# Kernel optimization log

Measured on AMD Instinct MI355X. Metric: run time of the kernel, lower is better.

## Reference

```python
import jax, jax.numpy as jnp
import numpy as np

C = 128
N_ATOMS = 3584          # 512 * 7 bands
DILATIONS = (1, 3, 9, 27, 81, 1)
NEG = 0.2               # leaky_relu slope used throughout the repo
B, T = 8, 2048


def lrelu(x):
    return jnp.where(x >= 0, x, NEG * x)


def setup_inputs() -> dict:
    key = jax.random.key(0)
    keys = iter(jax.random.split(key, 40))

    def rn(shape, scale=0.05):
        return jax.random.normal(next(keys), shape, jnp.float32) * scale

    # x: [B, 4, T]; channel 0 = atom index (stored as float, cast with .long() in forward),
    # channels 1:3 = (pos, amp), channel 3 = band size (unused by forward)
    atoms = jax.random.randint(next(keys), (B, 1, T), 0, N_ATOMS).astype(jnp.float32)
    pos_amp = jax.random.normal(next(keys), (B, 2, T), jnp.float32)
    band = jnp.zeros((B, 1, T), jnp.float32)
    x = jnp.concatenate([atoms, pos_amp, band], axis=1)

    nl = len(DILATIONS)
    return {
        "x": x,
        "embed_w": rn((N_ATOMS, C), 0.1),
        "posamp_w": rn((C, 2), 0.1), "posamp_b": jnp.zeros((C,), jnp.float32),
        "reduce_w": rn((C, 2 * C)), "reduce_b": jnp.zeros((C,), jnp.float32),
        "dil_w": rn((nl, C, C, 3)), "dil_b": jnp.zeros((nl, C), jnp.float32),
        "one_w": rn((nl, C, C)), "one_b": jnp.zeros((nl, C), jnp.float32),
        "atom_w1": rn((C, C)), "atom_b1": jnp.zeros((C,), jnp.float32),
        "atom_w2": rn((C, C)), "atom_b2": jnp.zeros((C,), jnp.float32),
        "atom_w3": rn((N_ATOMS, C)), "atom_b3": jnp.zeros((N_ATOMS,), jnp.float32),
        "pa_w1": rn((C, C)), "pa_b1": jnp.zeros((C,), jnp.float32),
        "pa_w2": rn((C, C)), "pa_b2": jnp.zeros((C,), jnp.float32),
        "pa_w3": rn((2, C)), "pa_b3": jnp.zeros((2,), jnp.float32),
    }


def _linear_stack(h, w1, b1, w2, b2, w3, b3):
    # LinearOutputStack(channels, 3, out_channels=...): two hidden linears with
    # leaky_relu, final linear with no activation.
    h = lrelu(h @ w1.T + b1)
    h = lrelu(h @ w2.T + b2)
    return h @ w3.T + b3


def reference(x, embed_w, posamp_w, posamp_b, reduce_w, reduce_b,
              dil_w, dil_b, one_w, one_b,
              atom_w1, atom_b1, atom_w2, atom_b2, atom_w3, atom_b3,
              pa_w1, pa_b1, pa_w2, pa_b2, pa_w3, pa_b3):
    xt = jnp.transpose(x, (0, 2, 1))                              # [B,T,4]
    idx = jax.lax.stop_gradient(xt[:, :, 0]).astype(jnp.int32)    # atom ids
    at = embed_w[idx]                                             # [B,T,C] gather
    pa = xt[:, :, 1:3] @ posamp_w.T + posamp_b                    # [B,T,C]
    h = jnp.concatenate([at, pa], axis=-1)                        # [B,T,2C]
    h = h @ reduce_w.T + reduce_b                                 # 1x1 conv == linear
    h = jnp.transpose(h, (0, 2, 1))                               # [B,C,T]

    # DilatedStack: residual blocks (dilated k=3 conv -> 1x1 conv -> +res -> lrelu)
    for i, d in enumerate(DILATIONS):
        orig = h
        y = jax.lax.conv_general_dilated(
            h, dil_w[i], window_strides=(1,), padding=[(d, d)],
            rhs_dilation=(d,), dimension_numbers=('NCH', 'OIH', 'NCH'))
        y = y + dil_b[i][None, :, None]
        y = jnp.einsum('oc,bct->bot', one_w[i], y) + one_b[i][None, :, None]
        h = lrelu(y + orig)

    ht = jnp.transpose(h, (0, 2, 1))                              # [B,T,C]
    # Original applies the output stacks over all T, then slices the last step.
    a = _linear_stack(ht, atom_w1, atom_b1, atom_w2, atom_b2, atom_w3, atom_b3)[:, -1:, :]
    pa_out = _linear_stack(ht, pa_w1, pa_b1, pa_w2, pa_b2, pa_w3, pa_b3)[:, -1:, :]
    return a, pa_out
```

## Files before the change

### kernel.cpp

```cpp
#include <hip/hip_runtime.h>

#define CCH 128
#define TLEN 2048
#define NBATCH 8
#define NATOMS 3584
#define NEG 0.2f
typedef unsigned long long ull;

#define PK1(a) ((ull)(a))
#define PK2(a,b) (PK1(a)|((ull)(b)<<7))
#define PK3(a,b,c) (PK2(a,b)|((ull)(c)<<14))
#define PK4(a,b,c,d) (PK3(a,b,c)|((ull)(d)<<21))
#define PK5(a,b,c,d,e) (PK4(a,b,c,d)|((ull)(e)<<28))
#define P6(v,k) ((ull)(v)<<(6*(k)))
#define PX10(a,b,c,d,e,f,g,h,i,j) (P6(a,0)|P6(b,1)|P6(c,2)|P6(d,3)|P6(e,4)| \
    P6(f,5)|P6(g,6)|P6(h,7)|P6(i,8)|P6(j,9))

__device__ const int g_l2cols[28] = {
    9,10,18,19,27,28,36,37,45,46,54,55,63,64,
    72,73,81,82,90,91,99,100,108,109,117,118,126,127};

__device__ __forceinline__ float lrelu(float v) { return v >= 0.f ? v : NEG * v; }
__device__ __forceinline__ float dot4(float4 w, float4 x) {
    return w.x * x.x + w.y * x.y + w.z * x.z + w.w * x.w;
}

__device__ __forceinline__ void warm(const float* p, int nf4, int gid, int nthr) {
    const float4* q = (const float4*)p;
    for (int i = gid; i < nf4; i += nthr) {
        float4 v = q[i];
        asm volatile("" :: "v"(v.x), "v"(v.y), "v"(v.z), "v"(v.w));
    }
}

__device__ __forceinline__ float red16x4(float a0, float a1, float a2, float a3, int s) {
    a0 += __shfl_xor(a0, 8); a1 += __shfl_xor(a1, 8);
    a2 += __shfl_xor(a2, 8); a3 += __shfl_xor(a3, 8);
    a0 += __shfl_xor(a0, 4); a1 += __shfl_xor(a1, 4);
    a2 += __shfl_xor(a2, 4); a3 += __shfl_xor(a3, 4);
    float u0 = (s & 2) ? a2 : a0;
    float v0 = (s & 2) ? a0 : a2;
    u0 += __shfl_xor(v0, 2);
    float u1 = (s & 2) ? a3 : a1;
    float v1 = (s & 2) ? a1 : a3;
    u1 += __shfl_xor(v1, 2);
    float w  = (s & 1) ? u1 : u0;
    float vv = (s & 1) ? u0 : u1;
    w += __shfl_xor(vv, 1);
    return w;
}

template<int NB, int SH = 7>
__device__ __forceinline__ void conv4(
        const float (*src)[CCH], float (*dst)[CCH], float* gout,
        ull pm, ull pc, ull pp, ull pd, int a0,
        const float* __restrict__ Wd, const float* __restrict__ bd,
        const float* __restrict__ Wo, const float* __restrict__ bo,
        float (*ybuf)[CCH], int g, int s)
{
    const int MSK = (1 << SH) - 1;
    const int ch = 4 * g + (s & 3);
    const float myBd = bd[ch];
    const float myBo = bo[ch];
    float4 W[24], V[8];
    {
        const float4* Wr = (const float4*)Wd + (size_t)(4 * g) * 96;
        #pragma unroll
        for (int r = 0; r < 4; ++r)
            #pragma unroll
            for (int j = 0; j < 3; ++j) {
                W[r * 6 + j]     = Wr[r * 96 + 3 * s + j];
                W[r * 6 + 3 + j] = Wr[r * 96 + 3 * s + 48 + j];
            }
        const float4* Or = (const float4*)Wo + (size_t)(4 * g) * 32;
        #pragma unroll
        for (int r = 0; r < 4; ++r) {
            V[r * 2]     = Or[r * 32 + s];
            V[r * 2 + 1] = Or[r * 32 + s + 16];
        }
    }
    __syncthreads();
    #pragma unroll
    for (int t = 0; t < NB; ++t) {
        const float* fm = src[(int)((pm >> (SH * t)) & MSK)];
        const float* fc = src[(int)((pc >> (SH * t)) & MSK)];
        const float* fp = src[(int)((pp >> (SH * t)) & MSK)];
        float4 m0 = *(const float4*)(fm + 4 * s);
        float4 m1 = *(const float4*)(fm + 4 * s + 64);
        float4 c0 = *(const float4*)(fc + 4 * s);
        float4 c1 = *(const float4*)(fc + 4 * s + 64);
        float4 p0 = *(const float4*)(fp + 4 * s);
        float4 p1 = *(const float4*)(fp + 4 * s + 64);
        float acc[4];
        #pragma unroll
        for (int r = 0; r < 4; ++r) {
            float4 wA = W[r*6+0], wB = W[r*6+1], wC = W[r*6+2];
            float a = wA.x*m0.x + wA.y*c0.x + wA.z*p0.x + wA.w*m0.y
                    + wB.x*c0.y + wB.y*p0.y + wB.z*m0.z + wB.w*c0.z
                    + wC.x*p0.z + wC.y*m0.w + wC.z*c0.w + wC.w*p0.w;
            float4 wD = W[r*6+3], wE = W[r*6+4], wF = W[r*6+5];
            float b2 = wD.x*m1.x + wD.y*c1.x + wD.z*p1.x + wD.w*m1.y
                     + wE.x*c1.y + wE.y*p1.y + wE.z*m1.z + wE.w*c1.z
                     + wF.x*p1.z + wF.y*m1.w + wF.z*c1.w + wF.w*p1.w;
            acc[r] = a + b2;
        }
        float tot = red16x4(acc[0], acc[1], acc[2], acc[3], s);
        if (s < 4) ybuf[t][ch] = tot + myBd;
    }
    __syncthreads();
    #pragma unroll
    for (int t = 0; t < NB; ++t) {
        int jc = (int)((pc >> (SH * t)) & MSK);
        int jd = (int)((pd >> (SH * t)) & MSK);
        const float* y = ybuf[t];
        float4 y0 = *(const float4*)(y + 4 * s);
        float4 y1 = *(const float4*)(y + 4 * s + 64);
        float a0_ = dot4(V[0], y0) + dot4(V[1], y1);
        float a1_ = dot4(V[2], y0) + dot4(V[3], y1);
        float a2_ = dot4(V[4], y0) + dot4(V[5], y1);
        float a3_ = dot4(V[6], y0) + dot4(V[7], y1);
        float tot = red16x4(a0_, a1_, a2_, a3_, s);
        if (s < 4) {
            float h = lrelu(tot + myBo + src[jc][ch]);
            if (gout) gout[ch] = h;
            else      dst[jd][ch] = (a0 + jd < 128) ? h : 0.f;
        }
    }
}

__device__ __forceinline__ void mlp4(
        const float* hin, float* hout,
        const float* __restrict__ w, const float* __restrict__ bv,
        int g, int s)
{
    const int ch = 4 * g + (s & 3);
    const float myB = bv[ch];
    float4 V[8];
    const float4* r = (const float4*)w + (size_t)(4 * g) * 32;
    #pragma unroll
    for (int rr = 0; rr < 4; ++rr) {
        V[rr * 2]     = r[rr * 32 + s];
        V[rr * 2 + 1] = r[rr * 32 + s + 16];
    }
    __syncthreads();
    float4 x0 = *(const float4*)(hin + 4 * s);
    float4 x1 = *(const float4*)(hin + 4 * s + 64);
    float a0_ = dot4(V[0], x0) + dot4(V[1], x1);
    float a1_ = dot4(V[2], x0) + dot4(V[3], x1);
    float a2_ = dot4(V[4], x0) + dot4(V[5], x1);
    float a3_ = dot4(V[6], x0) + dot4(V[7], x1);
    float tot = red16x4(a0_, a1_, a2_, a3_, s);
    if (s < 4) hout[ch] = lrelu(tot + myB);
}

__global__ void __launch_bounds__(512, 2) k_cone(
        const float* __restrict__ x,
        const float* __restrict__ embed_w,
        const float* __restrict__ posamp_w,
        const float* __restrict__ posamp_b,
        const float* __restrict__ reduce_w,
        const float* __restrict__ reduce_b,
        const float* __restrict__ dil_w,
        const float* __restrict__ dil_b,
        const float* __restrict__ one_w,
        const float* __restrict__ one_b,
        const float* __restrict__ aw1, const float* __restrict__ aw2,
        const float* __restrict__ pw1, const float* __restrict__ pw2,
        const float* __restrict__ aw3,
        float* __restrict__ l2c)
{
    const int i   = blockIdx.x;
    const int b   = blockIdx.y;
    const int own = g_l2cols[i];
    const int a0  = own - 4;
    const int tid = threadIdx.x;
    const int g   = tid >> 4;
    const int s   = tid & 15;
    const int ch  = 4 * g + (s & 3);

    {
        const int gid  = (b * 28 + i) * 512 + tid;
        const int nthr = 224 * 512;
        warm(dil_w + (size_t)2 * CCH * CCH * 3, 4 * CCH * CCH * 3 / 4, gid, nthr);
        warm(one_w + (size_t)2 * CCH * CCH,     4 * CCH * CCH / 4,     gid, nthr);
        warm(aw1, CCH * CCH / 4, gid, nthr);
        warm(aw2, CCH * CCH / 4, gid, nthr);
        warm(pw1, CCH * CCH / 4, gid, nthr);
        warm(pw2, CCH * CCH / 4, gid, nthr);
        warm(aw3, NATOMS * CCH / 4, gid, nthr);
    }

    __shared__ float A[9][CCH];
    __shared__ float B[8][CCH];
    __shared__ float cat[9][2 * CCH];
    __shared__ float ybuf[3][CCH];

    const float* xb = x + b * 4 * TLEN;
    for (int v = tid; v < 9 * 256; v += 512) {
        int p   = v >> 8;
        int chv = v & 255;
        int ab  = a0 + p;
        float val = 0.f;
        if (ab < 128) {
            int t = (TLEN - 128) + ab;
            if (chv < CCH) {
                int idx = (int)xb[t];
                val = embed_w[idx * CCH + chv];
            } else {
                int cc = chv - CCH;
                val = posamp_w[2 * cc] * xb[TLEN + t]
                    + posamp_w[2 * cc + 1] * xb[2 * TLEN + t] + posamp_b[cc];
            }
        }
        cat[p][chv] = val;
    }
    float4 RW[16];
    const float4* rw = (const float4*)reduce_w + (size_t)(4 * g) * 64;
    #pragma unroll
    for (int r = 0; r < 4; ++r)
        #pragma unroll
        for (int j = 0; j < 4; ++j)
            RW[r * 4 + j] = rw[r * 64 + s + 16 * j];
    const float rb = reduce_b[ch];
    __syncthreads();

    #pragma unroll 3
    for (int t = 0; t < 9; ++t) {
        const float* sc = cat[t];
        float4 x0 = *(const float4*)(sc + 4 * s);
        float4 x1 = *(const float4*)(sc + 4 * s + 64);
        float4 x2 = *(const float4*)(sc + 4 * s + 128);
        float4 x3 = *(const float4*)(sc + 4 * s + 192);
        float a0_ = dot4(RW[0], x0) + dot4(RW[1], x1) + dot4(RW[2], x2) + dot4(RW[3], x3);
        float a1_ = dot4(RW[4], x0) + dot4(RW[5], x1) + dot4(RW[6], x2) + dot4(RW[7], x3);
        float a2_ = dot4(RW[8], x0) + dot4(RW[9], x1) + dot4(RW[10], x2) + dot4(RW[11], x3);
        float a3_ = dot4(RW[12], x0) + dot4(RW[13], x1) + dot4(RW[14], x2) + dot4(RW[15], x3);
        float tot = red16x4(a0_, a1_, a2_, a3_, s);
        if (s < 4) A[t][ch] = (a0 + t < 128) ? tot + rb : 0.f;
    }

    conv4<3>(A, B, nullptr,
             PK3(0,3,6), PK3(1,4,7), PK3(2,5,8), PK3(1,4,7), a0,
             dil_w, dil_b, one_w, one_b, ybuf, g, s);
    conv4<1>(B, B, l2c + (size_t)(b * 28 + i) * CCH,
             PK1(1), PK1(4), PK1(7), PK1(4), a0,
             dil_w + (size_t)1 * CCH * CCH * 3, dil_b + CCH,
             one_w + (size_t)1 * CCH * CCH, one_b + CCH, ybuf, g, s);
}

__global__ void __launch_bounds__(512, 2) k_tail(
        const float* __restrict__ l2c,
        const float* __restrict__ dil_w,
        const float* __restrict__ dil_b,
        const float* __restrict__ one_w,
        const float* __restrict__ one_b,
        const float* __restrict__ aw1, const float* __restrict__ ab1,
        const float* __restrict__ aw2, const float* __restrict__ ab2,
        const float* __restrict__ aw3, const float* __restrict__ ab3,
        const float* __restrict__ pw1, const float* __restrict__ pb1,
        const float* __restrict__ pw2, const float* __restrict__ pb2,
        const float* __restrict__ pw3, const float* __restrict__ pb3,
        float* __restrict__ out)
{
    const int g2  = blockIdx.x;
    const int b   = blockIdx.y;
    const int tid = threadIdx.x;
    const int g   = tid >> 4;
    const int s   = tid & 15;

    __shared__ float E[29][CCH];
    __shared__ float D[11][CCH];
    __shared__ float B2[5][CCH];
    __shared__ float C2[3][CCH];
    __shared__ float HF[CCH];
    __shared__ float ybuf[10][CCH];
    __shared__ float h1a[CCH], h2a[CCH], h1p[CCH], h2p[CCH];

    if (tid < CCH) { E[28][tid] = 0.f; D[10][tid] = 0.f; B2[4][tid] = 0.f; C2[2][tid] = 0.f; }
    for (int v = tid; v < 28 * 32; v += 512) {
        int col = v >> 5, f4i = v & 31;
        *(float4*)&E[col][f4i * 4] =
            *(const float4*)(l2c + (size_t)(b * 28 + col) * CCH + f4i * 4);
    }

    conv4<10, 6>(E, D, nullptr,
             PX10(0,1,6,7,12,13,18,19,24,25),
             PX10(2,3,8,9,14,15,20,21,26,27),
             PX10(4,5,10,11,16,17,22,23,28,28),
             PX10(0,1,2,3,4,5,6,7,8,9), -1000,
             dil_w + (size_t)2 * CCH * CCH * 3, dil_b + 2 * CCH,
             one_w + (size_t)2 * CCH * CCH, one_b + 2 * CCH, ybuf, g, s);

    conv4<4>(D, B2, nullptr,
             PK4(0,1,6,7), PK4(2,3,8,9), PK4(4,5,10,10), PK4(0,1,2,3), -1000,
             dil_w + (size_t)3 * CCH * CCH * 3, dil_b + 3 * CCH,
             one_w + (size_t)3 * CCH * CCH, one_b + 3 * CCH, ybuf, g, s);
    conv4<2>(B2, C2, nullptr,
             PK2(0,1), PK2(2,3), PK2(4,4), PK2(0,1), -1000,
             dil_w + (size_t)4 * CCH * CCH * 3, dil_b + 4 * CCH,
             one_w + (size_t)4 * CCH * CCH, one_b + 4 * CCH, ybuf, g, s);
    conv4<1>(C2, C2, HF,
             PK1(0), PK1(1), PK1(2), PK1(0), -1000,
             dil_w + (size_t)5 * CCH * CCH * 3, dil_b + 5 * CCH,
             one_w + (size_t)5 * CCH * CCH, one_b + 5 * CCH, ybuf, g, s);

    mlp4(HF, h1a, aw1, ab1, g, s);
    mlp4(HF, h1p, pw1, pb1, g, s);
    mlp4(h1a, h2a, aw2, ab2, g, s);
    mlp4(h1p, h2p, pw2, pb2, g, s);
    __syncthreads();

    if (tid < 448) {
        int row = g2 * 448 + tid;
        const float4* r = (const float4*)(aw3 + (size_t)row * CCH);
        float s0 = 0.f, s1 = 0.f, s2 = 0.f, s3 = 0.f;
        #pragma unroll
        for (int k = 0; k < 32; k += 4) {
            s0 += dot4(r[k],     *(const float4*)&h2a[4 * k]);
            s1 += dot4(r[k + 1], *(const float4*)&h2a[4 * k + 4]);
            s2 += dot4(r[k + 2], *(const float4*)&h2a[4 * k + 8]);
            s3 += dot4(r[k + 3], *(const float4*)&h2a[4 * k + 12]);
        }
        out[b * NATOMS + row] = s0 + s1 + s2 + s3 + ab3[row];
    } else if (g2 == 0 && tid >= 448 && tid < 448 + 64) {
        int q = tid - 448;
        int row = q >> 5, qq = q & 31;
        float4 w4 = *(const float4*)(pw3 + row * CCH + 4 * qq);
        float4 xv = *(const float4*)(h2p + 4 * qq);
        float acc = dot4(w4, xv);
        acc += __shfl_xor(acc, 1);
        acc += __shfl_xor(acc, 2);
        acc += __shfl_xor(acc, 4);
        acc += __shfl_xor(acc, 8);
        acc += __shfl_xor(acc, 16);
        if (qq == 0) out[NBATCH * NATOMS + b * 2 + row] = acc + pb3[row];
    }
}

extern "C" void kernel_launch(void* const* d_in, const int* in_sizes, int n_in,
                              void* d_out, int out_size, void* d_ws, size_t ws_size,
                              hipStream_t stream)
{
    const float* x        = (const float*)d_in[0];
    const float* embed_w  = (const float*)d_in[1];
    const float* posamp_w = (const float*)d_in[2];
    const float* posamp_b = (const float*)d_in[3];
    const float* reduce_w = (const float*)d_in[4];
    const float* reduce_b = (const float*)d_in[5];
    const float* dil_w    = (const float*)d_in[6];
    const float* dil_b    = (const float*)d_in[7];
    const float* one_w    = (const float*)d_in[8];
    const float* one_b    = (const float*)d_in[9];
    const float* aw1 = (const float*)d_in[10]; const float* ab1 = (const float*)d_in[11];
    const float* aw2 = (const float*)d_in[12]; const float* ab2 = (const float*)d_in[13];
    const float* aw3 = (const float*)d_in[14]; const float* ab3 = (const float*)d_in[15];
    const float* pw1 = (const float*)d_in[16]; const float* pb1 = (const float*)d_in[17];
    const float* pw2 = (const float*)d_in[18]; const float* pb2 = (const float*)d_in[19];
    const float* pw3 = (const float*)d_in[20]; const float* pb3 = (const float*)d_in[21];

    float* l2c = (float*)d_ws;

    k_cone<<<dim3(28, NBATCH), dim3(512), 0, stream>>>(
        x, embed_w, posamp_w, posamp_b, reduce_w, reduce_b,
        dil_w, dil_b, one_w, one_b,
        aw1, aw2, pw1, pw2, aw3, l2c);

    k_tail<<<dim3(8, NBATCH), dim3(512), 0, stream>>>(
        l2c, dil_w, dil_b, one_w, one_b,
        aw1, ab1, aw2, ab2, aw3, ab3,
        pw1, pb1, pw2, pb2, pw3, pb3, (float*)d_out);
}
```

Before: 52.47 us.

## Run atom and pos-amp MLP layers concurrently and prefetch more weights

Replaces the four sequential per-stack MLP layer calls with two dual calls. In each call half the block computes the atom stack and half the pos-amp stack, each thread handling 16 float4 weights with an 8-lane shuffle reduction. This removes two barrier-separated phases from the tail kernel's serial chain. It also warms reduce_w and the first two dilation layers' weights in k_cone, and has each k_tail block prefetch its slice of aw3 at the start. Launch bounds drop from 2 to 1 blocks per CU, which frees registers for the larger per-thread weight arrays but may lower occupancy.

Measured after the change: 55.19 us. 1.05x slower.

```diff
diff --git a/kernel.cpp b/kernel.cpp
--- a/kernel.cpp
+++ b/kernel.cpp
@@ -11,7 +11,6 @@
 #define PK2(a,b) (PK1(a)|((ull)(b)<<7))
 #define PK3(a,b,c) (PK2(a,b)|((ull)(c)<<14))
 #define PK4(a,b,c,d) (PK3(a,b,c)|((ull)(d)<<21))
-#define PK5(a,b,c,d,e) (PK4(a,b,c,d)|((ull)(e)<<28))
 #define P6(v,k) ((ull)(v)<<(6*(k)))
 #define PX10(a,b,c,d,e,f,g,h,i,j) (P6(a,0)|P6(b,1)|P6(c,2)|P6(d,3)|P6(e,4)| \
     P6(f,5)|P6(g,6)|P6(h,7)|P6(i,8)|P6(j,9))
@@ -128,32 +127,53 @@
     }
 }
 
-__device__ __forceinline__ void mlp4(
-        const float* hin, float* hout,
-        const float* __restrict__ w, const float* __restrict__ bv,
-        int g, int s)
-{
-    const int ch = 4 * g + (s & 3);
-    const float myB = bv[ch];
-    float4 V[8];
-    const float4* r = (const float4*)w + (size_t)(4 * g) * 32;
+__device__ __forceinline__ void mlp4dual(
+        const float* hinA, const float* hinP,
+        float* houtA, float* houtP,
+        const float* __restrict__ wa, const float* __restrict__ ba,
+        const float* __restrict__ wp, const float* __restrict__ bp,
+        int tid)
+{
+    const int s8  = tid & 7;
+    const int g64 = tid >> 3;
+    const int sel = g64 >> 5;
+    const int gi  = g64 & 31;
+    const int ch  = 4 * gi + (s8 & 3);
+    const float* w   = sel ? wp : wa;
+    const float myB  = (sel ? bp : ba)[ch];
+    const float* hin = sel ? hinP : hinA;
+    float* hout      = sel ? houtP : houtA;
+    float4 V[16];
+    const float4* r = (const float4*)w + (size_t)(4 * gi) * 32;
     #pragma unroll
-    for (int rr = 0; rr < 4; ++rr) {
-        V[rr * 2]     = r[rr * 32 + s];
-        V[rr * 2 + 1] = r[rr * 32 + s + 16];
-    }
-    __syncthreads();
-    float4 x0 = *(const float4*)(hin + 4 * s);
-    float4 x1 = *(const float4*)(hin + 4 * s + 64);
-    float a0_ = dot4(V[0], x0) + dot4(V[1], x1);
-    float a1_ = dot4(V[2], x0) + dot4(V[3], x1);
-    float a2_ = dot4(V[4], x0) + dot4(V[5], x1);
-    float a3_ = dot4(V[6], x0) + dot4(V[7], x1);
-    float tot = red16x4(a0_, a1_, a2_, a3_, s);
-    if (s < 4) hout[ch] = lrelu(tot + myB);
-}
-
-__global__ void __launch_bounds__(512, 2) k_cone(
+    for (int rr = 0; rr < 4; ++rr)
+        #pragma unroll
+        for (int j = 0; j < 4; ++j)
+            V[rr * 4 + j] = r[rr * 32 + s8 + 8 * j];
+    __syncthreads();
+    float4 x0 = *(const float4*)(hin + 4 * s8);
+    float4 x1 = *(const float4*)(hin + 4 * s8 + 32);
+    float4 x2 = *(const float4*)(hin + 4 * s8 + 64);
+    float4 x3 = *(const float4*)(hin + 4 * s8 + 96);
+    float a0 = dot4(V[0],x0)+dot4(V[1],x1)+dot4(V[2],x2)+dot4(V[3],x3);
+    float a1 = dot4(V[4],x0)+dot4(V[5],x1)+dot4(V[6],x2)+dot4(V[7],x3);
+    float a2 = dot4(V[8],x0)+dot4(V[9],x1)+dot4(V[10],x2)+dot4(V[11],x3);
+    float a3 = dot4(V[12],x0)+dot4(V[13],x1)+dot4(V[14],x2)+dot4(V[15],x3);
+    a0 += __shfl_xor(a0, 4); a1 += __shfl_xor(a1, 4);
+    a2 += __shfl_xor(a2, 4); a3 += __shfl_xor(a3, 4);
+    float u0 = (s8 & 2) ? a2 : a0;
+    float v0 = (s8 & 2) ? a0 : a2;
+    u0 += __shfl_xor(v0, 2);
+    float u1 = (s8 & 2) ? a3 : a1;
+    float v1 = (s8 & 2) ? a1 : a3;
+    u1 += __shfl_xor(v1, 2);
+    float wv = (s8 & 1) ? u1 : u0;
+    float vv = (s8 & 1) ? u0 : u1;
+    wv += __shfl_xor(vv, 1);
+    if (s8 < 4) hout[ch] = lrelu(wv + myB);
+}
+
+__global__ void __launch_bounds__(512, 1) k_cone(
         const float* __restrict__ x,
         const float* __restrict__ embed_w,
         const float* __restrict__ posamp_w,
@@ -181,6 +201,9 @@
     {
         const int gid  = (b * 28 + i) * 512 + tid;
         const int nthr = 224 * 512;
+        warm(reduce_w, 2 * CCH * CCH / 4, gid, nthr);
+        warm(dil_w, 2 * CCH * CCH * 3 / 4, gid, nthr);
+        warm(one_w, 2 * CCH * CCH / 4, gid, nthr);
         warm(dil_w + (size_t)2 * CCH * CCH * 3, 4 * CCH * CCH * 3 / 4, gid, nthr);
         warm(one_w + (size_t)2 * CCH * CCH,     4 * CCH * CCH / 4,     gid, nthr);
         warm(aw1, CCH * CCH / 4, gid, nthr);
@@ -248,7 +271,7 @@
              one_w + (size_t)1 * CCH * CCH, one_b + CCH, ybuf, g, s);
 }
 
-__global__ void __launch_bounds__(512, 2) k_tail(
+__global__ void __launch_bounds__(512, 1) k_tail(
         const float* __restrict__ l2c,
         const float* __restrict__ dil_w,
         const float* __restrict__ dil_b,
@@ -268,6 +291,8 @@
     const int g   = tid >> 4;
     const int s   = tid & 15;
 
+    warm(aw3 + (size_t)g2 * 448 * CCH, 448 * CCH / 4, tid, 512);
+
     __shared__ float E[29][CCH];
     __shared__ float D[11][CCH];
     __shared__ float B2[5][CCH];
@@ -304,10 +329,8 @@
              dil_w + (size_t)5 * CCH * CCH * 3, dil_b + 5 * CCH,
              one_w + (size_t)5 * CCH * CCH, one_b + 5 * CCH, ybuf, g, s);
 
-    mlp4(HF, h1a, aw1, ab1, g, s);
-    mlp4(HF, h1p, pw1, pb1, g, s);
-    mlp4(h1a, h2a, aw2, ab2, g, s);
-    mlp4(h1p, h2p, pw2, pb2, g, s);
+    mlp4dual(HF,  HF,  h1a, h1p, aw1, ab1, pw1, pb1, tid);
+    mlp4dual(h1a, h1p, h2a, h2p, aw2, ab2, pw2, pb2, tid);
     __syncthreads();
 
     if (tid < 448) {
```

## Fuse cone and tail kernels into one launch with inter-block flag synchronization

Applied to the files above, without the earlier changes.

Merges the two kernels into a single persistent-style launch of 288 blocks. 224 blocks compute the per-batch cone columns, 8 per-batch tail blocks spin on atomic counters until their 28 columns are ready, and 56 further blocks wait for all tails before computing the large atom output projection across all batches. This removes the second kernel launch and kernel boundary, and spreads the final 3584-row projection over more blocks with pre-warmed weight slices. The cost is an extra memset, and the spin-waits depend on all 288 blocks being co-resident, which risks deadlock or idle spinning.

Measured after the change: 74.12 us. +41.3%, slower.

```diff
diff --git a/kernel.cpp b/kernel.cpp
--- a/kernel.cpp
+++ b/kernel.cpp
@@ -11,7 +11,6 @@
 #define PK2(a,b) (PK1(a)|((ull)(b)<<7))
 #define PK3(a,b,c) (PK2(a,b)|((ull)(c)<<14))
 #define PK4(a,b,c,d) (PK3(a,b,c)|((ull)(d)<<21))
-#define PK5(a,b,c,d,e) (PK4(a,b,c,d)|((ull)(e)<<28))
 #define P6(v,k) ((ull)(v)<<(6*(k)))
 #define PX10(a,b,c,d,e,f,g,h,i,j) (P6(a,0)|P6(b,1)|P6(c,2)|P6(d,3)|P6(e,4)| \
     P6(f,5)|P6(g,6)|P6(h,7)|P6(i,8)|P6(j,9))
@@ -153,187 +152,213 @@
     if (s < 4) hout[ch] = lrelu(tot + myB);
 }
 
-__global__ void __launch_bounds__(512, 2) k_cone(
-        const float* __restrict__ x,
-        const float* __restrict__ embed_w,
-        const float* __restrict__ posamp_w,
-        const float* __restrict__ posamp_b,
-        const float* __restrict__ reduce_w,
-        const float* __restrict__ reduce_b,
-        const float* __restrict__ dil_w,
-        const float* __restrict__ dil_b,
-        const float* __restrict__ one_w,
-        const float* __restrict__ one_b,
-        const float* __restrict__ aw1, const float* __restrict__ aw2,
-        const float* __restrict__ pw1, const float* __restrict__ pw2,
-        const float* __restrict__ aw3,
-        float* __restrict__ l2c)
+struct Params {
+    const float *x, *embed_w, *posamp_w, *posamp_b, *reduce_w, *reduce_b;
+    const float *dil_w, *dil_b, *one_w, *one_b;
+    const float *aw1, *ab1, *aw2, *ab2, *aw3, *ab3;
+    const float *pw1, *pb1, *pw2, *pb2, *pw3, *pb3;
+    float *l2c, *h2a;
+    int  *flags;
+    float *out;
+};
+
+__global__ void __launch_bounds__(512, 2) k_fused(Params P)
 {
-    const int i   = blockIdx.x;
-    const int b   = blockIdx.y;
-    const int own = g_l2cols[i];
-    const int a0  = own - 4;
+    __shared__ float smem[8192];
+    const int bid = blockIdx.x;
     const int tid = threadIdx.x;
     const int g   = tid >> 4;
     const int s   = tid & 15;
-    const int ch  = 4 * g + (s & 3);
-
-    {
-        const int gid  = (b * 28 + i) * 512 + tid;
-        const int nthr = 224 * 512;
-        warm(dil_w + (size_t)2 * CCH * CCH * 3, 4 * CCH * CCH * 3 / 4, gid, nthr);
-        warm(one_w + (size_t)2 * CCH * CCH,     4 * CCH * CCH / 4,     gid, nthr);
-        warm(aw1, CCH * CCH / 4, gid, nthr);
-        warm(aw2, CCH * CCH / 4, gid, nthr);
-        warm(pw1, CCH * CCH / 4, gid, nthr);
-        warm(pw2, CCH * CCH / 4, gid, nthr);
-        warm(aw3, NATOMS * CCH / 4, gid, nthr);
-    }
-
-    __shared__ float A[9][CCH];
-    __shared__ float B[8][CCH];
-    __shared__ float cat[9][2 * CCH];
-    __shared__ float ybuf[3][CCH];
-
-    const float* xb = x + b * 4 * TLEN;
-    for (int v = tid; v < 9 * 256; v += 512) {
-        int p   = v >> 8;
-        int chv = v & 255;
-        int ab  = a0 + p;
-        float val = 0.f;
-        if (ab < 128) {
-            int t = (TLEN - 128) + ab;
-            if (chv < CCH) {
-                int idx = (int)xb[t];
-                val = embed_w[idx * CCH + chv];
-            } else {
-                int cc = chv - CCH;
-                val = posamp_w[2 * cc] * xb[TLEN + t]
-                    + posamp_w[2 * cc + 1] * xb[2 * TLEN + t] + posamp_b[cc];
+
+    if (bid < 224) {
+        const int i   = bid % 28;
+        const int b   = bid / 28;
+        const int own = g_l2cols[i];
+        const int a0  = own - 4;
+        const int ch  = 4 * g + (s & 3);
+
+        {
+            const int gid  = bid * 512 + tid;
+            const int nthr = 224 * 512;
+            warm(P.reduce_w, 2 * CCH * CCH / 4, gid, nthr);
+            warm(P.dil_w, 2 * CCH * CCH * 3 / 4, gid, nthr);
+            warm(P.one_w, 2 * CCH * CCH / 4, gid, nthr);
+        }
+
+        float (*A)[CCH]      = (float(*)[CCH])(smem);
+        float (*B)[CCH]      = (float(*)[CCH])(smem + 1152);
+        float (*cat)[2*CCH]  = (float(*)[2*CCH])(smem + 2176);
+        float (*ybuf)[CCH]   = (float(*)[CCH])(smem + 4480);
+
+        const float* xb = P.x + b * 4 * TLEN;
+        for (int v = tid; v < 9 * 256; v += 512) {
+            int p   = v >> 8;
+            int chv = v & 255;
+            int ab  = a0 + p;
+            float val = 0.f;
+            if (ab < 128) {
+                int t = (TLEN - 128) + ab;
+                if (chv < CCH) {
+                    int idx = (int)xb[t];
+                    val = P.embed_w[idx * CCH + chv];
+                } else {
+                    int cc = chv - CCH;
+                    val = P.posamp_w[2 * cc] * xb[TLEN + t]
+                        + P.posamp_w[2 * cc + 1] * xb[2 * TLEN + t] + P.posamp_b[cc];
+                }
             }
-        }
-        cat[p][chv] = val;
-    }
-    float4 RW[16];
-    const float4* rw = (const float4*)reduce_w + (size_t)(4 * g) * 64;
-    #pragma unroll
-    for (int r = 0; r < 4; ++r)
-        #pragma unroll
-        for (int j = 0; j < 4; ++j)
-            RW[r * 4 + j] = rw[r * 64 + s + 16 * j];
-    const float rb = reduce_b[ch];
-    __syncthreads();
-
-    #pragma unroll 3
-    for (int t = 0; t < 9; ++t) {
-        const float* sc = cat[t];
-        float4 x0 = *(const float4*)(sc + 4 * s);
-        float4 x1 = *(const float4*)(sc + 4 * s + 64);
-        float4 x2 = *(const float4*)(sc + 4 * s + 128);
-        float4 x3 = *(const float4*)(sc + 4 * s + 192);
-        float a0_ = dot4(RW[0], x0) + dot4(RW[1], x1) + dot4(RW[2], x2) + dot4(RW[3], x3);
-        float a1_ = dot4(RW[4], x0) + dot4(RW[5], x1) + dot4(RW[6], x2) + dot4(RW[7], x3);
-        float a2_ = dot4(RW[8], x0) + dot4(RW[9], x1) + dot4(RW[10], x2) + dot4(RW[11], x3);
-        float a3_ = dot4(RW[12], x0) + dot4(RW[13], x1) + dot4(RW[14], x2) + dot4(RW[15], x3);
-        float tot = red16x4(a0_, a1_, a2_, a3_, s);
-        if (s < 4) A[t][ch] = (a0 + t < 128) ? tot + rb : 0.f;
-    }
-
-    conv4<3>(A, B, nullptr,
-             PK3(0,3,6), PK3(1,4,7), PK3(2,5,8), PK3(1,4,7), a0,
-             dil_w, dil_b, one_w, one_b, ybuf, g, s);
-    conv4<1>(B, B, l2c + (size_t)(b * 28 + i) * CCH,
-             PK1(1), PK1(4), PK1(7), PK1(4), a0,
-             dil_w + (size_t)1 * CCH * CCH * 3, dil_b + CCH,
-             one_w + (size_t)1 * CCH * CCH, one_b + CCH, ybuf, g, s);
-}
-
-__global__ void __launch_bounds__(512, 2) k_tail(
-        const float* __restrict__ l2c,
-        const float* __restrict__ dil_w,
-        const float* __restrict__ dil_b,
-        const float* __restrict__ one_w,
-        const float* __restrict__ one_b,
-        const float* __restrict__ aw1, const float* __restrict__ ab1,
-        const float* __restrict__ aw2, const float* __restrict__ ab2,
-        const float* __restrict__ aw3, const float* __restrict__ ab3,
-        const float* __restrict__ pw1, const float* __restrict__ pb1,
-        const float* __restrict__ pw2, const float* __restrict__ pb2,
-        const float* __restrict__ pw3, const float* __restrict__ pb3,
-        float* __restrict__ out)
-{
-    const int g2  = blockIdx.x;
-    const int b   = blockIdx.y;
-    const int tid = threadIdx.x;
-    const int g   = tid >> 4;
-    const int s   = tid & 15;
-
-    __shared__ float E[29][CCH];
-    __shared__ float D[11][CCH];
-    __shared__ float B2[5][CCH];
-    __shared__ float C2[3][CCH];
-    __shared__ float HF[CCH];
-    __shared__ float ybuf[10][CCH];
-    __shared__ float h1a[CCH], h2a[CCH], h1p[CCH], h2p[CCH];
-
-    if (tid < CCH) { E[28][tid] = 0.f; D[10][tid] = 0.f; B2[4][tid] = 0.f; C2[2][tid] = 0.f; }
-    for (int v = tid; v < 28 * 32; v += 512) {
-        int col = v >> 5, f4i = v & 31;
-        *(float4*)&E[col][f4i * 4] =
-            *(const float4*)(l2c + (size_t)(b * 28 + col) * CCH + f4i * 4);
-    }
-
-    conv4<10, 6>(E, D, nullptr,
-             PX10(0,1,6,7,12,13,18,19,24,25),
-             PX10(2,3,8,9,14,15,20,21,26,27),
-             PX10(4,5,10,11,16,17,22,23,28,28),
-             PX10(0,1,2,3,4,5,6,7,8,9), -1000,
-             dil_w + (size_t)2 * CCH * CCH * 3, dil_b + 2 * CCH,
-             one_w + (size_t)2 * CCH * CCH, one_b + 2 * CCH, ybuf, g, s);
-
-    conv4<4>(D, B2, nullptr,
-             PK4(0,1,6,7), PK4(2,3,8,9), PK4(4,5,10,10), PK4(0,1,2,3), -1000,
-             dil_w + (size_t)3 * CCH * CCH * 3, dil_b + 3 * CCH,
-             one_w + (size_t)3 * CCH * CCH, one_b + 3 * CCH, ybuf, g, s);
-    conv4<2>(B2, C2, nullptr,
-             PK2(0,1), PK2(2,3), PK2(4,4), PK2(0,1), -1000,
-             dil_w + (size_t)4 * CCH * CCH * 3, dil_b + 4 * CCH,
-             one_w + (size_t)4 * CCH * CCH, one_b + 4 * CCH, ybuf, g, s);
-    conv4<1>(C2, C2, HF,
-             PK1(0), PK1(1), PK1(2), PK1(0), -1000,
-             dil_w + (size_t)5 * CCH * CCH * 3, dil_b + 5 * CCH,
-             one_w + (size_t)5 * CCH * CCH, one_b + 5 * CCH, ybuf, g, s);
-
-    mlp4(HF, h1a, aw1, ab1, g, s);
-    mlp4(HF, h1p, pw1, pb1, g, s);
-    mlp4(h1a, h2a, aw2, ab2, g, s);
-    mlp4(h1p, h2p, pw2, pb2, g, s);
-    __syncthreads();
-
-    if (tid < 448) {
-        int row = g2 * 448 + tid;
-        const float4* r = (const float4*)(aw3 + (size_t)row * CCH);
+            cat[p][chv] = val;
+        }
+        float4 RW[16];
+        const float4* rw = (const float4*)P.reduce_w + (size_t)(4 * g) * 64;
+        #pragma unroll
+        for (int r = 0; r < 4; ++r)
+            #pragma unroll
+            for (int j = 0; j < 4; ++j)
+                RW[r * 4 + j] = rw[r * 64 + s + 16 * j];
+        const float rb = P.reduce_b[ch];
+        __syncthreads();
+
+        #pragma unroll 3
+        for (int t = 0; t < 9; ++t) {
+            const float* sc = cat[t];
+            float4 x0 = *(const float4*)(sc + 4 * s);
+            float4 x1 = *(const float4*)(sc + 4 * s + 64);
+            float4 x2 = *(const float4*)(sc + 4 * s + 128);
+            float4 x3 = *(const float4*)(sc + 4 * s + 192);
+            float a0_ = dot4(RW[0],x0)+dot4(RW[1],x1)+dot4(RW[2],x2)+dot4(RW[3],x3);
+            float a1_ = dot4(RW[4],x0)+dot4(RW[5],x1)+dot4(RW[6],x2)+dot4(RW[7],x3);
+            float a2_ = dot4(RW[8],x0)+dot4(RW[9],x1)+dot4(RW[10],x2)+dot4(RW[11],x3);
+            float a3_ = dot4(RW[12],x0)+dot4(RW[13],x1)+dot4(RW[14],x2)+dot4(RW[15],x3);
+            float tot = red16x4(a0_, a1_, a2_, a3_, s);
+            if (s < 4) A[t][ch] = (a0 + t < 128) ? tot + rb : 0.f;
+        }
+
+        conv4<3>(A, B, nullptr,
+                 PK3(0,3,6), PK3(1,4,7), PK3(2,5,8), PK3(1,4,7), a0,
+                 P.dil_w, P.dil_b, P.one_w, P.one_b, ybuf, g, s);
+        conv4<1>(B, B, P.l2c + (size_t)(b * 28 + i) * CCH,
+                 PK1(1), PK1(4), PK1(7), PK1(4), a0,
+                 P.dil_w + (size_t)1 * CCH * CCH * 3, P.dil_b + CCH,
+                 P.one_w + (size_t)1 * CCH * CCH, P.one_b + CCH, ybuf, g, s);
+
+        __syncthreads();
+        if (tid == 0) {
+            __threadfence();
+            __hip_atomic_fetch_add(&P.flags[b], 1, __ATOMIC_RELAXED,
+                                   __HIP_MEMORY_SCOPE_AGENT);
+        }
+    } else if (bid < 232) {
+        const int b = bid - 224;
+
+        warm(P.dil_w + (size_t)2 * CCH * CCH * 3, 4 * CCH * CCH * 3 / 4, tid, 512);
+        warm(P.one_w + (size_t)2 * CCH * CCH,     4 * CCH * CCH / 4,     tid, 512);
+        warm(P.aw1, CCH * CCH / 4, tid, 512);
+        warm(P.aw2, CCH * CCH / 4, tid, 512);
+        warm(P.pw1, CCH * CCH / 4, tid, 512);
+        warm(P.pw2, CCH * CCH / 4, tid, 512);
+
+        if (tid == 0) {
+            while (__hip_atomic_load(&P.flags[b], __ATOMIC_RELAXED,
+                                     __HIP_MEMORY_SCOPE_AGENT) < 28)
+                __builtin_amdgcn_s_sleep(2);
+            __threadfence();
+        }
+        __syncthreads();
+
+        float (*E)[CCH]    = (float(*)[CCH])(smem);
+        float (*D)[CCH]    = (float(*)[CCH])(smem + 3712);
+        float (*B2)[CCH]   = (float(*)[CCH])(smem + 5120);
+        float (*C2)[CCH]   = (float(*)[CCH])(smem + 5760);
+        float* HF          = smem + 6144;
+        float (*ybuf)[CCH] = (float(*)[CCH])(smem + 6272);
+        float* h1a         = smem + 7552;
+        float* h1p         = smem + 7680;
+        float* h2p         = smem + 7808;
+
+        if (tid < CCH) { E[28][tid] = 0.f; D[10][tid] = 0.f; B2[4][tid] = 0.f; C2[2][tid] = 0.f; }
+        for (int v = tid; v < 28 * 32; v += 512) {
+            int col = v >> 5, f4i = v & 31;
+            *(float4*)&E[col][f4i * 4] =
+                *(const float4*)(P.l2c + (size_t)(b * 28 + col) * CCH + f4i * 4);
+        }
+
+        conv4<10, 6>(E, D, nullptr,
+                 PX10(0,1,6,7,12,13,18,19,24,25),
+                 PX10(2,3,8,9,14,15,20,21,26,27),
+                 PX10(4,5,10,11,16,17,22,23,28,28),
+                 PX10(0,1,2,3,4,5,6,7,8,9), -1000,
+                 P.dil_w + (size_t)2 * CCH * CCH * 3, P.dil_b + 2 * CCH,
+                 P.one_w + (size_t)2 * CCH * CCH, P.one_b + 2 * CCH, ybuf, g, s);
+        conv4<4>(D, B2, nullptr,
+                 PK4(0,1,6,7), PK4(2,3,8,9), PK4(4,5,10,10), PK4(0,1,2,3), -1000,
+                 P.dil_w + (size_t)3 * CCH * CCH * 3, P.dil_b + 3 * CCH,
+                 P.one_w + (size_t)3 * CCH * CCH, P.one_b + 3 * CCH, ybuf, g, s);
+        conv4<2>(B2, C2, nullptr,
+                 PK2(0,1), PK2(2,3), PK2(4,4), PK2(0,1), -1000,
+                 P.dil_w + (size_t)4 * CCH * CCH * 3, P.dil_b + 4 * CCH,
+                 P.one_w + (size_t)4 * CCH * CCH, P.one_b + 4 * CCH, ybuf, g, s);
+        conv4<1>(C2, C2, HF,
+                 PK1(0), PK1(1), PK1(2), PK1(0), -1000,
+                 P.dil_w + (size_t)5 * CCH * CCH * 3, P.dil_b + 5 * CCH,
+                 P.one_w + (size_t)5 * CCH * CCH, P.one_b + 5 * CCH, ybuf, g, s);
+
+        mlp4(HF,  h1a, P.aw1, P.ab1, g, s);
+        mlp4(HF,  h1p, P.pw1, P.pb1, g, s);
+        mlp4(h1a, P.h2a + b * CCH, P.aw2, P.ab2, g, s);
+        mlp4(h1p, h2p, P.pw2, P.pb2, g, s);
+        __syncthreads();
+
+        if (tid < 64) {
+            int row = tid >> 5, q = tid & 31;
+            float4 w4 = *(const float4*)(P.pw3 + row * CCH + 4 * q);
+            float4 xv = *(const float4*)(h2p + 4 * q);
+            float acc = dot4(w4, xv);
+            acc += __shfl_xor(acc, 1);
+            acc += __shfl_xor(acc, 2);
+            acc += __shfl_xor(acc, 4);
+            acc += __shfl_xor(acc, 8);
+            acc += __shfl_xor(acc, 16);
+            if (q == 0) P.out[NBATCH * NATOMS + b * 2 + row] = acc + P.pb3[row];
+        }
+        __syncthreads();
+        if (tid == 0) {
+            __threadfence();
+            __hip_atomic_fetch_add(&P.flags[8], 1, __ATOMIC_RELAXED,
+                                   __HIP_MEMORY_SCOPE_AGENT);
+        }
+    } else {
+        const int j = bid - 232;
+
+        warm(P.aw3 + (size_t)j * 64 * CCH, 64 * CCH / 4, tid, 512);
+
+        if (tid == 0) {
+            while (__hip_atomic_load(&P.flags[8], __ATOMIC_RELAXED,
+                                     __HIP_MEMORY_SCOPE_AGENT) < 8)
+                __builtin_amdgcn_s_sleep(2);
+            __threadfence();
+        }
+        __syncthreads();
+
+        float (*hs)[CCH] = (float(*)[CCH])smem;
+        if (tid < 256)
+            ((float4*)hs)[tid] = ((const float4*)P.h2a)[tid];
+        __syncthreads();
+
+        const int b   = tid >> 6;
+        const int r   = tid & 63;
+        const int row = j * 64 + r;
+        const float4* wr = (const float4*)(P.aw3 + (size_t)row * CCH);
+        const float*  h  = hs[b];
         float s0 = 0.f, s1 = 0.f, s2 = 0.f, s3 = 0.f;
         #pragma unroll
         for (int k = 0; k < 32; k += 4) {
-            s0 += dot4(r[k],     *(const float4*)&h2a[4 * k]);
-            s1 += dot4(r[k + 1], *(const float4*)&h2a[4 * k + 4]);
-            s2 += dot4(r[k + 2], *(const float4*)&h2a[4 * k + 8]);
-            s3 += dot4(r[k + 3], *(const float4*)&h2a[4 * k + 12]);
-        }
-        out[b * NATOMS + row] = s0 + s1 + s2 + s3 + ab3[row];
-    } else if (g2 == 0 && tid >= 448 && tid < 448 + 64) {
-        int q = tid - 448;
-        int row = q >> 5, qq = q & 31;
-        float4 w4 = *(const float4*)(pw3 + row * CCH + 4 * qq);
-        float4 xv = *(const float4*)(h2p + 4 * qq);
-        float acc = dot4(w4, xv);
-        acc += __shfl_xor(acc, 1);
-        acc += __shfl_xor(acc, 2);
-        acc += __shfl_xor(acc, 4);
-        acc += __shfl_xor(acc, 8);
-        acc += __shfl_xor(acc, 16);
-        if (qq == 0) out[NBATCH * NATOMS + b * 2 + row] = acc + pb3[row];
+            s0 += dot4(wr[k],     *(const float4*)&h[4 * k]);
+            s1 += dot4(wr[k + 1], *(const float4*)&h[4 * k + 4]);
+            s2 += dot4(wr[k + 2], *(const float4*)&h[4 * k + 8]);
+            s3 += dot4(wr[k + 3], *(const float4*)&h[4 * k + 12]);
+        }
+        P.out[b * NATOMS + row] = s0 + s1 + s2 + s3 + P.ab3[row];
     }
 }
 
@@ -341,32 +366,30 @@
                               void* d_out, int out_size, void* d_ws, size_t ws_size,
                               hipStream_t stream)
 {
-    const float* x        = (const float*)d_in[0];
-    const float* embed_w  = (const float*)d_in[1];
-    const float* posamp_w = (const float*)d_in[2];
-    const float* posamp_b = (const float*)d_in[3];
-    const float* reduce_w = (const float*)d_in[4];
-    const float* reduce_b = (const float*)d_in[5];
-    const float* dil_w    = (const float*)d_in[6];
-    const float* dil_b    = (const float*)d_in[7];
-    const float* one_w    = (const float*)d_in[8];
-    const float* one_b    = (const float*)d_in[9];
-    const float* aw1 = (const float*)d_in[10]; const float* ab1 = (const float*)d_in[11];
-    const float* aw2 = (const float*)d_in[12]; const float* ab2 = (const float*)d_in[13];
-    const float* aw3 = (const float*)d_in[14]; const float* ab3 = (const float*)d_in[15];
-    const float* pw1 = (const float*)d_in[16]; const float* pb1 = (const float*)d_in[17];
-    const float* pw2 = (const float*)d_in[18]; const float* pb2 = (const float*)d_in[19];
-    const float* pw3 = (const float*)d_in[20]; const float* pb3 = (const float*)d_in[21];
-
-    float* l2c = (float*)d_ws;
-
-    k_cone<<<dim3(28, NBATCH), dim3(512), 0, stream>>>(
-        x, embed_w, posamp_w, posamp_b, reduce_w, reduce_b,
-        dil_w, dil_b, one_w, one_b,
-        aw1, aw2, pw1, pw2, aw3, l2c);
-
-    k_tail<<<dim3(8, NBATCH), dim3(512), 0, stream>>>(
-        l2c, dil_w, dil_b, one_w, one_b,
-        aw1, ab1, aw2, ab2, aw3, ab3,
-        pw1, pb1, pw2, pb2, pw3, pb3, (float*)d_out);
-}
+    Params P;
+    P.x        = (const float*)d_in[0];
+    P.embed_w  = (const float*)d_in[1];
+    P.posamp_w = (const float*)d_in[2];
+    P.posamp_b = (const float*)d_in[3];
+    P.reduce_w = (const float*)d_in[4];
+    P.reduce_b = (const float*)d_in[5];
+    P.dil_w    = (const float*)d_in[6];
+    P.dil_b    = (const float*)d_in[7];
+    P.one_w    = (const float*)d_in[8];
+    P.one_b    = (const float*)d_in[9];
+    P.aw1 = (const float*)d_in[10]; P.ab1 = (const float*)d_in[11];
+    P.aw2 = (const float*)d_in[12]; P.ab2 = (const float*)d_in[13];
+    P.aw3 = (const float*)d_in[14]; P.ab3 = (const float*)d_in[15];
+    P.pw1 = (const float*)d_in[16]; P.pb1 = (const float*)d_in[17];
+    P.pw2 = (const float*)d_in[18]; P.pb2 = (const float*)d_in[19];
+    P.pw3 = (const float*)d_in[20]; P.pb3 = (const float*)d_in[21];
+
+    char* ws = (char*)d_ws;
+    P.flags = (int*)ws;
+    P.l2c   = (float*)(ws + 256);
+    P.h2a   = P.l2c + NBATCH * 28 * CCH;
+    P.out   = (float*)d_out;
+
+    hipMemsetAsync(d_ws, 0, 256, stream);
+    k_fused<<<dim3(288), dim3(512), 0, stream>>>(P);
+}
```

## Split atom output projection into separate batched head kernel sharing weights

Applied to the files above, without the earlier changes.

The tail kernel now runs one block per batch instead of eight replicated blocks per batch. Each block writes its second hidden atom activation to workspace. A new k_head kernel then computes the 3584x128 atom projection for all eight batches at once, so each aw3 row is read once and reused across batches instead of being streamed eight times. This removes the redundant tail convolution work and the repeated weight traffic, at the cost of an extra kernel launch and a global round trip for the hidden vector.

After: 54.84 us. +4.5%, slower.

```diff
diff --git a/kernel.cpp b/kernel.cpp
--- a/kernel.cpp
+++ b/kernel.cpp
@@ -11,7 +11,6 @@
 #define PK2(a,b) (PK1(a)|((ull)(b)<<7))
 #define PK3(a,b,c) (PK2(a,b)|((ull)(c)<<14))
 #define PK4(a,b,c,d) (PK3(a,b,c)|((ull)(d)<<21))
-#define PK5(a,b,c,d,e) (PK4(a,b,c,d)|((ull)(e)<<28))
 #define P6(v,k) ((ull)(v)<<(6*(k)))
 #define PX10(a,b,c,d,e,f,g,h,i,j) (P6(a,0)|P6(b,1)|P6(c,2)|P6(d,3)|P6(e,4)| \
     P6(f,5)|P6(g,6)|P6(h,7)|P6(i,8)|P6(j,9))
@@ -256,14 +255,13 @@
         const float* __restrict__ one_b,
         const float* __restrict__ aw1, const float* __restrict__ ab1,
         const float* __restrict__ aw2, const float* __restrict__ ab2,
-        const float* __restrict__ aw3, const float* __restrict__ ab3,
         const float* __restrict__ pw1, const float* __restrict__ pb1,
         const float* __restrict__ pw2, const float* __restrict__ pb2,
         const float* __restrict__ pw3, const float* __restrict__ pb3,
+        float* __restrict__ h2w,
         float* __restrict__ out)
 {
-    const int g2  = blockIdx.x;
-    const int b   = blockIdx.y;
+    const int b   = blockIdx.x;
     const int tid = threadIdx.x;
     const int g   = tid >> 4;
     const int s   = tid & 15;
@@ -274,7 +272,7 @@
     __shared__ float C2[3][CCH];
     __shared__ float HF[CCH];
     __shared__ float ybuf[10][CCH];
-    __shared__ float h1a[CCH], h2a[CCH], h1p[CCH], h2p[CCH];
+    __shared__ float h1a[CCH], h1p[CCH], h2p[CCH];
 
     if (tid < CCH) { E[28][tid] = 0.f; D[10][tid] = 0.f; B2[4][tid] = 0.f; C2[2][tid] = 0.f; }
     for (int v = tid; v < 28 * 32; v += 512) {
@@ -290,7 +288,6 @@
              PX10(0,1,2,3,4,5,6,7,8,9), -1000,
              dil_w + (size_t)2 * CCH * CCH * 3, dil_b + 2 * CCH,
              one_w + (size_t)2 * CCH * CCH, one_b + 2 * CCH, ybuf, g, s);
-
     conv4<4>(D, B2, nullptr,
              PK4(0,1,6,7), PK4(2,3,8,9), PK4(4,5,10,10), PK4(0,1,2,3), -1000,
              dil_w + (size_t)3 * CCH * CCH * 3, dil_b + 3 * CCH,
@@ -304,37 +301,53 @@
              dil_w + (size_t)5 * CCH * CCH * 3, dil_b + 5 * CCH,
              one_w + (size_t)5 * CCH * CCH, one_b + 5 * CCH, ybuf, g, s);
 
-    mlp4(HF, h1a, aw1, ab1, g, s);
-    mlp4(HF, h1p, pw1, pb1, g, s);
-    mlp4(h1a, h2a, aw2, ab2, g, s);
+    mlp4(HF,  h1a, aw1, ab1, g, s);
+    mlp4(HF,  h1p, pw1, pb1, g, s);
+    mlp4(h1a, h2w + b * CCH, aw2, ab2, g, s);
     mlp4(h1p, h2p, pw2, pb2, g, s);
     __syncthreads();
 
-    if (tid < 448) {
-        int row = g2 * 448 + tid;
-        const float4* r = (const float4*)(aw3 + (size_t)row * CCH);
-        float s0 = 0.f, s1 = 0.f, s2 = 0.f, s3 = 0.f;
-        #pragma unroll
-        for (int k = 0; k < 32; k += 4) {
-            s0 += dot4(r[k],     *(const float4*)&h2a[4 * k]);
-            s1 += dot4(r[k + 1], *(const float4*)&h2a[4 * k + 4]);
-            s2 += dot4(r[k + 2], *(const float4*)&h2a[4 * k + 8]);
-            s3 += dot4(r[k + 3], *(const float4*)&h2a[4 * k + 12]);
-        }
-        out[b * NATOMS + row] = s0 + s1 + s2 + s3 + ab3[row];
-    } else if (g2 == 0 && tid >= 448 && tid < 448 + 64) {
-        int q = tid - 448;
-        int row = q >> 5, qq = q & 31;
-        float4 w4 = *(const float4*)(pw3 + row * CCH + 4 * qq);
-        float4 xv = *(const float4*)(h2p + 4 * qq);
+    if (tid < 64) {
+        int row = tid >> 5, q = tid & 31;
+        float4 w4 = *(const float4*)(pw3 + row * CCH + 4 * q);
+        float4 xv = *(const float4*)(h2p + 4 * q);
         float acc = dot4(w4, xv);
         acc += __shfl_xor(acc, 1);
         acc += __shfl_xor(acc, 2);
         acc += __shfl_xor(acc, 4);
         acc += __shfl_xor(acc, 8);
         acc += __shfl_xor(acc, 16);
-        if (qq == 0) out[NBATCH * NATOMS + b * 2 + row] = acc + pb3[row];
-    }
+        if (q == 0) out[NBATCH * NATOMS + b * 2 + row] = acc + pb3[row];
+    }
+}
+
+__global__ void __launch_bounds__(512, 2) k_head(
+        const float* __restrict__ h2w,
+        const float* __restrict__ aw3, const float* __restrict__ ab3,
+        float* __restrict__ out)
+{
+    const int j   = blockIdx.x;
+    const int tid = threadIdx.x;
+
+    __shared__ float hs[NBATCH][CCH];
+    if (tid < 256)
+        ((float4*)hs)[tid] = ((const float4*)h2w)[tid];
+    __syncthreads();
+
+    const int b   = tid >> 6;
+    const int r   = tid & 63;
+    const int row = j * 64 + r;
+    const float4* wr = (const float4*)(aw3 + (size_t)row * CCH);
+    const float*  h  = hs[b];
+    float s0 = 0.f, s1 = 0.f, s2 = 0.f, s3 = 0.f;
+    #pragma unroll
+    for (int k = 0; k < 32; k += 4) {
+        s0 += dot4(wr[k],     *(const float4*)&h[4 * k]);
+        s1 += dot4(wr[k + 1], *(const float4*)&h[4 * k + 4]);
+        s2 += dot4(wr[k + 2], *(const float4*)&h[4 * k + 8]);
+        s3 += dot4(wr[k + 3], *(const float4*)&h[4 * k + 12]);
+    }
+    out[b * NATOMS + row] = s0 + s1 + s2 + s3 + ab3[row];
 }
 
 extern "C" void kernel_launch(void* const* d_in, const int* in_sizes, int n_in,
@@ -359,14 +372,18 @@
     const float* pw3 = (const float*)d_in[20]; const float* pb3 = (const float*)d_in[21];
 
     float* l2c = (float*)d_ws;
+    float* h2w = l2c + NBATCH * 28 * CCH;
 
     k_cone<<<dim3(28, NBATCH), dim3(512), 0, stream>>>(
         x, embed_w, posamp_w, posamp_b, reduce_w, reduce_b,
         dil_w, dil_b, one_w, one_b,
         aw1, aw2, pw1, pw2, aw3, l2c);
 
-    k_tail<<<dim3(8, NBATCH), dim3(512), 0, stream>>>(
+    k_tail<<<dim3(NBATCH), dim3(512), 0, stream>>>(
         l2c, dil_w, dil_b, one_w, one_b,
-        aw1, ab1, aw2, ab2, aw3, ab3,
-        pw1, pb1, pw2, pb2, pw3, pb3, (float*)d_out);
-}
+        aw1, ab1, aw2, ab2, pw1, pb1, pw2, pb2, pw3, pb3,
+        h2w, (float*)d_out);
+
+    k_head<<<dim3(56), dim3(512), 0, stream>>>(
+        h2w, aw3, ab3, (float*)d_out);
+}
```
